# Kernel tuning notes

Measured on AMD Instinct MI355X. Metric: run time of the kernel, lower is better.

The kernel has to match this reference:

```python
import jax, jax.numpy as jnp
import numpy as np
import math

B, S, D = 16, 2048, 128
MASK_SENTINEL = -100

def setup_inputs() -> dict:
    key = jax.random.key(0)
    k1, k2, k3, k4 = jax.random.split(key, 4)
    value = jax.random.normal(k1, (B, S, D), dtype=jnp.float32)
    key_t = jax.random.normal(k2, (B, S, D), dtype=jnp.float32)
    query = jax.random.normal(k3, (B, S, D), dtype=jnp.float32)
    # mask uses -100 as the "masked out" sentinel, anything else is kept.
    bits = jax.random.randint(k4, (B, S, S), 0, 2, dtype=jnp.int32)
    mask = jnp.where(bits == 0, jnp.int32(MASK_SENTINEL), jnp.int32(0))
    return {"value": value, "key": key_t, "query": query, "mask": mask}

def reference(value, key, query, mask):
    # scores: [B, Sq, Sk]
    scale = 1.0 / math.sqrt(query.shape[-1])
    scores = jnp.einsum("bqd,bkd->bqk", query, key) * scale
    min_val = jnp.finfo(scores.dtype).min
    masked = jnp.where(mask == MASK_SENTINEL, min_val, scores)
    attn = jax.nn.softmax(masked, axis=-1)
    return jnp.einsum("bqk,bkd->bqd", attn, value)
```

## Files before the change

kernel.cpp:

```cpp
#include <hip/hip_runtime.h>
#include <hip/hip_bf16.h>

#define BATCH 16
#define SEQ   2048
#define DIM   128
#define QBLK  64
#define KVBLK 64
#define NT    (SEQ / KVBLK)
#define PPAD  72
#define L2E   1.4426950408889634f
#define THR   8.0f
#define MSENT -100

typedef __attribute__((ext_vector_type(8))) short bf16x8;
typedef __attribute__((ext_vector_type(4))) short bf16x4;
typedef __attribute__((ext_vector_type(4))) float f32x4;
typedef __attribute__((ext_vector_type(4))) unsigned u32x4;

__device__ __forceinline__ unsigned short f2bf(float f) {
  union { float f; unsigned u; } v; v.f = f;
  return (unsigned short)((v.u + 0x7FFFu + ((v.u >> 16) & 1u)) >> 16);
}
__device__ __forceinline__ unsigned packbf(float a, float b) {
  return ((unsigned)f2bf(b) << 16) | (unsigned)f2bf(a);
}

__global__ __launch_bounds__(256) void cvt_k(const float* __restrict__ K,
                                             short* __restrict__ Kb) {
  const size_t i = ((size_t)blockIdx.x * 256 + threadIdx.x) * 8;
  f32x4 a = __builtin_nontemporal_load((const f32x4*)(K + i));
  f32x4 b = __builtin_nontemporal_load((const f32x4*)(K + i + 4));
  u32x4 o = { packbf(a[0], a[1]), packbf(a[2], a[3]),
              packbf(b[0], b[1]), packbf(b[2], b[3]) };
  *(u32x4*)(Kb + i) = o;
}

__global__ __launch_bounds__(256) void cvt_vt(const float* __restrict__ V,
                                              short* __restrict__ Vt) {
  __shared__ unsigned t32[64][65];
  const int tid = threadIdx.x;
  const int b  = blockIdx.x >> 5;
  const int s0 = (blockIdx.x & 31) * 64;
  #pragma unroll
  for (int it = 0; it < 8; ++it) {
    const int idx = tid + it * 256;
    const int r = idx >> 5, c4 = idx & 31;
    f32x4 x = __builtin_nontemporal_load(
        (const f32x4*)(V + ((size_t)b * SEQ + s0 + r) * DIM + c4 * 4));
    t32[r][c4 * 2]     = packbf(x[0], x[1]);
    t32[r][c4 * 2 + 1] = packbf(x[2], x[3]);
  }
  __syncthreads();
  const int d = tid >> 1, sh = tid & 1;
  unsigned short outv[32];
  #pragma unroll
  for (int j = 0; j < 32; ++j) {
    const unsigned u = t32[sh * 32 + j][d >> 1];
    outv[j] = (d & 1) ? (unsigned short)(u >> 16) : (unsigned short)(u & 0xffff);
  }
  short* op = Vt + ((size_t)b * DIM + d) * SEQ + s0 + sh * 32;
  #pragma unroll
  for (int q = 0; q < 4; ++q) {
    bf16x8 y;
    #pragma unroll
    for (int j = 0; j < 8; ++j) y[j] = (short)outv[q * 8 + j];
    *(bf16x8*)(op + q * 8) = y;
  }
}

__device__ __forceinline__ void gload16(const void* g, void* l) {
  __builtin_amdgcn_global_load_lds(
      (const __attribute__((address_space(1))) unsigned*)g,
      (__attribute__((address_space(3))) unsigned*)l, 16, 0, 0);
}

__device__ __forceinline__ void stage_kv(const char* __restrict__ Kb2,
                                         const char* __restrict__ Vtb2,
                                         int k0, int w, int l,
                                         short* kbuf, short* vbuf) {
  #pragma unroll
  for (int it = 0; it < 4; ++it) {
    const int ch = w * 4 + it;
    const int r  = ch * 4 + (l >> 4);
    const int cs = ((l & 15) * 16) ^ ((r & 7) << 4);
    gload16(Kb2 + (size_t)(k0 + r) * 256 + cs, (char*)kbuf + ch * 1024);
  }
  #pragma unroll
  for (int it = 0; it < 4; ++it) {
    const int ch = w * 4 + it;
    const int d  = ch * 8 + (l >> 3);
    const int cs = ((l & 7) * 16) ^ ((d & 7) << 4);
    gload16(Vtb2 + (size_t)d * (SEQ * 2) + k0 * 2 + cs, (char*)vbuf + ch * 1024);
  }
}

__global__ __launch_bounds__(256, 2) void attn_fwd(
    const short* __restrict__ Kbf, const short* __restrict__ Vt,
    const float* __restrict__ Qg, const int* __restrict__ Mg,
    float* __restrict__ Og) {
  __shared__ short lds_k[2][KVBLK * DIM];
  __shared__ short lds_v[2][DIM * KVBLK];
  __shared__ short lds_p[4][16 * PPAD];

  const int tid = threadIdx.x;
  const int w   = tid >> 6;
  const int l   = tid & 63;
  const int g   = l >> 4;
  const int lr  = l & 15;

  const int blk = blockIdx.x;
  const int b   = blk >> 5;
  const int q0  = (blk & 31) * QBLK;

  const float scale = 0.08838834764831845f;

  const char* Kb2  = (const char*)(Kbf + (size_t)b * SEQ * DIM);
  const char* Vtb2 = (const char*)(Vt  + (size_t)b * DIM * SEQ);
  const int*  Mb   = Mg + (size_t)b * SEQ * SEQ;
  const int* const Mrow[4] = {
    Mb + (size_t)(q0 + w * 16 + 4 * g + 0) * SEQ + lr,
    Mb + (size_t)(q0 + w * 16 + 4 * g + 1) * SEQ + lr,
    Mb + (size_t)(q0 + w * 16 + 4 * g + 2) * SEQ + lr,
    Mb + (size_t)(q0 + w * 16 + 4 * g + 3) * SEQ + lr };

  stage_kv(Kb2, Vtb2, 0, w, l, lds_k[0], lds_v[0]);
  int mreg[16];
  #pragma unroll
  for (int sub = 0; sub < 4; ++sub)
    #pragma unroll
    for (int i = 0; i < 4; ++i)
      mreg[sub * 4 + i] = __builtin_nontemporal_load(Mrow[i] + sub * 16);

  bf16x8 qa[4];
  {
    const float* qbase = Qg + ((size_t)b * SEQ + (size_t)(q0 + w * 16 + lr)) * DIM + g * 8;
    #pragma unroll
    for (int kk = 0; kk < 4; ++kk) {
      f32x4 x0 = *(const f32x4*)(qbase + kk * 32);
      f32x4 x1 = *(const f32x4*)(qbase + kk * 32 + 4);
      bf16x8 f;
      #pragma unroll
      for (int j = 0; j < 4; ++j) {
        f[j]     = (short)f2bf(x0[j] * scale);
        f[j + 4] = (short)f2bf(x1[j] * scale);
      }
      qa[kk] = f;
    }
  }

  f32x4 acc[8];
  #pragma unroll
  for (int t = 0; t < 8; ++t) acc[t] = (f32x4){0.f, 0.f, 0.f, 0.f};
  float mrow[4] = {-1e30f, -1e30f, -1e30f, -1e30f};
  float lsum[4] = {0.f, 0.f, 0.f, 0.f};

  __syncthreads();
  int cur = 0;

  for (int t = 0; t < NT; ++t) {
    const int k0 = t * KVBLK;
    if (t + 1 < NT)
      stage_kv(Kb2, Vtb2, k0 + KVBLK, w, l, lds_k[cur ^ 1], lds_v[cur ^ 1]);

    const char* kbuf = (const char*)lds_k[cur];
    const char* vbuf = (const char*)lds_v[cur];

    f32x4 s[4];
    #pragma unroll
    for (int sub = 0; sub < 4; ++sub) {
      f32x4 sv = (f32x4){0.f, 0.f, 0.f, 0.f};
      const int krow = sub * 16 + lr;
      #pragma unroll
      for (int kk = 0; kk < 4; ++kk) {
        const int cb = (kk * 64 + g * 16) ^ ((krow & 7) << 4);
        bf16x8 kb = *(const bf16x8*)(kbuf + krow * 256 + cb);
        sv = __builtin_amdgcn_mfma_f32_16x16x32_bf16(qa[kk], kb, sv, 0, 0, 0);
      }
      s[sub] = sv;
    }

    #pragma unroll
    for (int sub = 0; sub < 4; ++sub)
      #pragma unroll
      for (int i = 0; i < 4; ++i)
        if (mreg[sub * 4 + i] == MSENT) s[sub][i] = -1e30f;
    if (t + 1 < NT) {
      #pragma unroll
      for (int sub = 0; sub < 4; ++sub)
        #pragma unroll
        for (int i = 0; i < 4; ++i)
          mreg[sub * 4 + i] =
              __builtin_nontemporal_load(Mrow[i] + k0 + KVBLK + sub * 16);
    }

    float tmax[4];
    bool chg = false;
    #pragma unroll
    for (int i = 0; i < 4; ++i) {
      float tm = fmaxf(fmaxf(s[0][i], s[1][i]), fmaxf(s[2][i], s[3][i]));
      #pragma unroll
      for (int dlt = 1; dlt < 16; dlt <<= 1)
        tm = fmaxf(tm, __shfl_xor(tm, dlt, 16));
      tmax[i] = tm;
      chg = chg || (tm > mrow[i] + THR);
    }
    if (__any(chg)) {
      #pragma unroll
      for (int i = 0; i < 4; ++i) {
        const float mnew = fmaxf(mrow[i], tmax[i]);
        const float alpha = __builtin_amdgcn_exp2f((mrow[i] - mnew) * L2E);
        mrow[i] = mnew;
        lsum[i] *= alpha;
        #pragma unroll
        for (int t8 = 0; t8 < 8; ++t8) acc[t8][i] *= alpha;
      }
    }

    #pragma unroll
    for (int sub = 0; sub < 4; ++sub)
      #pragma unroll
      for (int i = 0; i < 4; ++i) {
        const float p = __builtin_amdgcn_exp2f((s[sub][i] - mrow[i]) * L2E);
        lsum[i] += p;
        lds_p[w][(4 * g + i) * PPAD + sub * 16 + lr] = (short)f2bf(p);
      }

    bf16x8 pa[2];
    #pragma unroll
    for (int kk = 0; kk < 2; ++kk)
      pa[kk] = *(const bf16x8*)&lds_p[w][lr * PPAD + kk * 32 + g * 8];
    #pragma unroll
    for (int t8 = 0; t8 < 8; ++t8) {
      const int d = 16 * t8 + lr;
      #pragma unroll
      for (int kk = 0; kk < 2; ++kk) {
        const int cb = (kk * 64 + g * 16) ^ ((d & 7) << 4);
        bf16x8 vb = *(const bf16x8*)(vbuf + d * 128 + cb);
        acc[t8] = __builtin_amdgcn_mfma_f32_16x16x32_bf16(pa[kk], vb, acc[t8], 0, 0, 0);
      }
    }

    __syncthreads();
    cur ^= 1;
  }

  float rden[4];
  #pragma unroll
  for (int i = 0; i < 4; ++i) {
    float sm = lsum[i];
    #pragma unroll
    for (int dlt = 1; dlt < 16; dlt <<= 1) sm += __shfl_xor(sm, dlt, 16);
    rden[i] = 1.f / sm;
  }
  float* ob = Og + ((size_t)b * SEQ + (size_t)(q0 + w * 16)) * DIM;
  #pragma unroll
  for (int t8 = 0; t8 < 8; ++t8)
    #pragma unroll
    for (int i = 0; i < 4; ++i)
      ob[(4 * g + i) * DIM + 16 * t8 + lr] = acc[t8][i] * rden[i];
}

extern "C" void kernel_launch(void* const* d_in, const int* in_sizes, int n_in,
                              void* d_out, int out_size, void* d_ws, size_t ws_size,
                              hipStream_t stream) {
  (void)in_sizes; (void)n_in; (void)out_size; (void)ws_size;
  const float* Vg = (const float*)d_in[0];
  const float* Kg = (const float*)d_in[1];
  const float* Qg = (const float*)d_in[2];
  const int*   Mg = (const int*)d_in[3];
  float* Og = (float*)d_out;

  short* Kbf = (short*)d_ws;
  short* Vt  = Kbf + (size_t)BATCH * SEQ * DIM;
  cvt_k<<<dim3(BATCH * SEQ * DIM / (8 * 256)), 256, 0, stream>>>(Kg, Kbf);
  cvt_vt<<<dim3(BATCH * (SEQ / 64)), 256, 0, stream>>>(Vg, Vt);
  attn_fwd<<<dim3(BATCH * (SEQ / QBLK)), 256, 0, stream>>>(Kbf, Vt, Qg, Mg, Og);
}
```

Baseline: 118.4 us.

## Transpose QK^T MFMA, vectorize mask loads, new LDS swizzle, block remap, finer waits

```diff
diff --git a/kernel.cpp b/kernel.cpp
--- a/kernel.cpp
+++ b/kernel.cpp
@@ -13,8 +13,8 @@
 #define MSENT -100
 
 typedef __attribute__((ext_vector_type(8))) short bf16x8;
-typedef __attribute__((ext_vector_type(4))) short bf16x4;
 typedef __attribute__((ext_vector_type(4))) float f32x4;
+typedef __attribute__((ext_vector_type(4))) int   i32x4;
 typedef __attribute__((ext_vector_type(4))) unsigned u32x4;
 
 __device__ __forceinline__ unsigned short f2bf(float f) {
@@ -77,20 +77,23 @@
 __device__ __forceinline__ void stage_kv(const char* __restrict__ Kb2,
                                          const char* __restrict__ Vtb2,
                                          int k0, int w, int l,
-                                         short* kbuf, short* vbuf) {
+                                         void* kbuf, void* vbuf) {
   #pragma unroll
   for (int it = 0; it < 4; ++it) {
     const int ch = w * 4 + it;
     const int r  = ch * 4 + (l >> 4);
-    const int cs = ((l & 15) * 16) ^ ((r & 7) << 4);
-    gload16(Kb2 + (size_t)(k0 + r) * 256 + cs, (char*)kbuf + ch * 1024);
+    const int sg = (l & 15) ^ (r & 15);
+    gload16(Kb2 + (size_t)(k0 + r) * 256 + sg * 16, (char*)kbuf + ch * 1024);
   }
   #pragma unroll
   for (int it = 0; it < 4; ++it) {
     const int ch = w * 4 + it;
-    const int d  = ch * 8 + (l >> 3);
-    const int cs = ((l & 7) * 16) ^ ((d & 7) << 4);
-    gload16(Vtb2 + (size_t)d * (SEQ * 2) + k0 * 2 + cs, (char*)vbuf + ch * 1024);
+    const int d2 = ch * 4 + (l >> 4);
+    const int Su = (l & 15) ^ (d2 & 15);
+    const int d  = 2 * d2 + (Su >> 3);
+    const int m  = Su & 7;
+    gload16(Vtb2 + (size_t)d * (SEQ * 2) + k0 * 2 + m * 16,
+            (char*)vbuf + ch * 1024);
   }
 }
 
@@ -109,27 +112,18 @@
   const int lr  = l & 15;
 
   const int blk = blockIdx.x;
-  const int b   = blk >> 5;
-  const int q0  = (blk & 31) * QBLK;
+  const int swz = (blk & 7) * 64 + (blk >> 3);
+  const int b   = swz >> 5;
+  const int q0  = (swz & 31) * QBLK;
 
   const float scale = 0.08838834764831845f;
 
   const char* Kb2  = (const char*)(Kbf + (size_t)b * SEQ * DIM);
   const char* Vtb2 = (const char*)(Vt  + (size_t)b * DIM * SEQ);
-  const int*  Mb   = Mg + (size_t)b * SEQ * SEQ;
-  const int* const Mrow[4] = {
-    Mb + (size_t)(q0 + w * 16 + 4 * g + 0) * SEQ + lr,
-    Mb + (size_t)(q0 + w * 16 + 4 * g + 1) * SEQ + lr,
-    Mb + (size_t)(q0 + w * 16 + 4 * g + 2) * SEQ + lr,
-    Mb + (size_t)(q0 + w * 16 + 4 * g + 3) * SEQ + lr };
+  const int*  Mr   = Mg + (size_t)b * SEQ * SEQ + (size_t)(q0 + w * 16 + lr) * SEQ;
 
   stage_kv(Kb2, Vtb2, 0, w, l, lds_k[0], lds_v[0]);
-  int mreg[16];
-  #pragma unroll
-  for (int sub = 0; sub < 4; ++sub)
-    #pragma unroll
-    for (int i = 0; i < 4; ++i)
-      mreg[sub * 4 + i] = __builtin_nontemporal_load(Mrow[i] + sub * 16);
+  __builtin_amdgcn_sched_barrier(0);
 
   bf16x8 qa[4];
   {
@@ -147,83 +141,90 @@
       qa[kk] = f;
     }
   }
+  __builtin_amdgcn_sched_barrier(0);
+
+  i32x4 mreg[4];
+  #pragma unroll
+  for (int sub = 0; sub < 4; ++sub)
+    mreg[sub] = __builtin_nontemporal_load((const i32x4*)(Mr + 16 * sub + 4 * g));
 
   f32x4 acc[8];
   #pragma unroll
   for (int t = 0; t < 8; ++t) acc[t] = (f32x4){0.f, 0.f, 0.f, 0.f};
-  float mrow[4] = {-1e30f, -1e30f, -1e30f, -1e30f};
-  float lsum[4] = {0.f, 0.f, 0.f, 0.f};
-
-  __syncthreads();
+  float mrow = -1e30f, lsum = 0.f;
+
+  asm volatile("s_waitcnt vmcnt(4)" ::: "memory");
+  __builtin_amdgcn_s_barrier();
+
   int cur = 0;
-
   for (int t = 0; t < NT; ++t) {
     const int k0 = t * KVBLK;
     if (t + 1 < NT)
       stage_kv(Kb2, Vtb2, k0 + KVBLK, w, l, lds_k[cur ^ 1], lds_v[cur ^ 1]);
+    __builtin_amdgcn_sched_barrier(0);
 
     const char* kbuf = (const char*)lds_k[cur];
     const char* vbuf = (const char*)lds_v[cur];
 
     f32x4 s[4];
     #pragma unroll
-    for (int sub = 0; sub < 4; ++sub) {
-      f32x4 sv = (f32x4){0.f, 0.f, 0.f, 0.f};
-      const int krow = sub * 16 + lr;
-      #pragma unroll
-      for (int kk = 0; kk < 4; ++kk) {
-        const int cb = (kk * 64 + g * 16) ^ ((krow & 7) << 4);
+    for (int sub = 0; sub < 4; ++sub) s[sub] = (f32x4){0.f, 0.f, 0.f, 0.f};
+    #pragma unroll
+    for (int kk = 0; kk < 4; ++kk) {
+      #pragma unroll
+      for (int sub = 0; sub < 4; ++sub) {
+        const int krow = sub * 16 + lr;
+        const int cb = (64 * kk + 16 * g) ^ (lr << 4);
         bf16x8 kb = *(const bf16x8*)(kbuf + krow * 256 + cb);
-        sv = __builtin_amdgcn_mfma_f32_16x16x32_bf16(qa[kk], kb, sv, 0, 0, 0);
-      }
-      s[sub] = sv;
+        s[sub] = __builtin_amdgcn_mfma_f32_16x16x32_bf16(kb, qa[kk], s[sub], 0, 0, 0);
+      }
     }
 
     #pragma unroll
     for (int sub = 0; sub < 4; ++sub)
       #pragma unroll
       for (int i = 0; i < 4; ++i)
-        if (mreg[sub * 4 + i] == MSENT) s[sub][i] = -1e30f;
+        if (mreg[sub][i] == MSENT) s[sub][i] = -1e30f;
     if (t + 1 < NT) {
       #pragma unroll
       for (int sub = 0; sub < 4; ++sub)
+        mreg[sub] = __builtin_nontemporal_load(
+            (const i32x4*)(Mr + k0 + KVBLK + 16 * sub + 4 * g));
+    }
+
+    float tm = -1e30f;
+    #pragma unroll
+    for (int sub = 0; sub < 4; ++sub)
+      #pragma unroll
+      for (int i = 0; i < 4; ++i) tm = fmaxf(tm, s[sub][i]);
+    tm = fmaxf(tm, __shfl_xor(tm, 16));
+    tm = fmaxf(tm, __shfl_xor(tm, 32));
+    if (__any(tm > mrow + THR)) {
+      const float mnew = fmaxf(mrow, tm);
+      const float al = __builtin_amdgcn_exp2f((mrow - mnew) * L2E);
+      mrow = mnew; lsum *= al;
+      float av[4];
+      #pragma unroll
+      for (int i = 0; i < 4; ++i) av[i] = __shfl(al, 4 * g + i);
+      #pragma unroll
+      for (int t8 = 0; t8 < 8; ++t8)
         #pragma unroll
-        for (int i = 0; i < 4; ++i)
-          mreg[sub * 4 + i] =
-              __builtin_nontemporal_load(Mrow[i] + k0 + KVBLK + sub * 16);
-    }
-
-    float tmax[4];
-    bool chg = false;
-    #pragma unroll
-    for (int i = 0; i < 4; ++i) {
-      float tm = fmaxf(fmaxf(s[0][i], s[1][i]), fmaxf(s[2][i], s[3][i]));
-      #pragma unroll
-      for (int dlt = 1; dlt < 16; dlt <<= 1)
-        tm = fmaxf(tm, __shfl_xor(tm, dlt, 16));
-      tmax[i] = tm;
-      chg = chg || (tm > mrow[i] + THR);
-    }
-    if (__any(chg)) {
-      #pragma unroll
-      for (int i = 0; i < 4; ++i) {
-        const float mnew = fmaxf(mrow[i], tmax[i]);
-        const float alpha = __builtin_amdgcn_exp2f((mrow[i] - mnew) * L2E);
-        mrow[i] = mnew;
-        lsum[i] *= alpha;
-        #pragma unroll
-        for (int t8 = 0; t8 < 8; ++t8) acc[t8][i] *= alpha;
-      }
-    }
-
-    #pragma unroll
-    for (int sub = 0; sub < 4; ++sub)
-      #pragma unroll
-      for (int i = 0; i < 4; ++i) {
-        const float p = __builtin_amdgcn_exp2f((s[sub][i] - mrow[i]) * L2E);
-        lsum[i] += p;
-        lds_p[w][(4 * g + i) * PPAD + sub * 16 + lr] = (short)f2bf(p);
-      }
+        for (int i = 0; i < 4; ++i) acc[t8][i] *= av[i];
+    }
+
+    {
+      unsigned* prow = (unsigned*)&lds_p[w][lr * PPAD];
+      #pragma unroll
+      for (int sub = 0; sub < 4; ++sub) {
+        const float p0 = __builtin_amdgcn_exp2f((s[sub][0] - mrow) * L2E);
+        const float p1 = __builtin_amdgcn_exp2f((s[sub][1] - mrow) * L2E);
+        const float p2 = __builtin_amdgcn_exp2f((s[sub][2] - mrow) * L2E);
+        const float p3 = __builtin_amdgcn_exp2f((s[sub][3] - mrow) * L2E);
+        lsum += (p0 + p1) + (p2 + p3);
+        prow[8 * sub + 2 * g]     = packbf(p0, p1);
+        prow[8 * sub + 2 * g + 1] = packbf(p2, p3);
+      }
+    }
 
     bf16x8 pa[2];
     #pragma unroll
@@ -231,33 +232,34 @@
       pa[kk] = *(const bf16x8*)&lds_p[w][lr * PPAD + kk * 32 + g * 8];
     #pragma unroll
     for (int t8 = 0; t8 < 8; ++t8) {
-      const int d = 16 * t8 + lr;
+      const int d2 = 8 * t8 + (lr >> 1);
       #pragma unroll
       for (int kk = 0; kk < 2; ++kk) {
-        const int cb = (kk * 64 + g * 16) ^ ((d & 7) << 4);
-        bf16x8 vb = *(const bf16x8*)(vbuf + d * 128 + cb);
+        const int S = ((lr & 1) * 8 + 4 * kk + g) ^ (d2 & 15);
+        bf16x8 vb = *(const bf16x8*)(vbuf + d2 * 256 + S * 16);
         acc[t8] = __builtin_amdgcn_mfma_f32_16x16x32_bf16(pa[kk], vb, acc[t8], 0, 0, 0);
       }
     }
 
-    __syncthreads();
+    if (t + 1 < NT) {
+      asm volatile("s_waitcnt vmcnt(4)" ::: "memory");
+      __builtin_amdgcn_s_barrier();
+    }
     cur ^= 1;
   }
 
-  float rden[4];
-  #pragma unroll
-  for (int i = 0; i < 4; ++i) {
-    float sm = lsum[i];
-    #pragma unroll
-    for (int dlt = 1; dlt < 16; dlt <<= 1) sm += __shfl_xor(sm, dlt, 16);
-    rden[i] = 1.f / sm;
-  }
+  lsum += __shfl_xor(lsum, 16);
+  lsum += __shfl_xor(lsum, 32);
+  const float rden = 1.f / lsum;
+  float rdv[4];
+  #pragma unroll
+  for (int i = 0; i < 4; ++i) rdv[i] = __shfl(rden, 4 * g + i);
   float* ob = Og + ((size_t)b * SEQ + (size_t)(q0 + w * 16)) * DIM;
   #pragma unroll
   for (int t8 = 0; t8 < 8; ++t8)
     #pragma unroll
     for (int i = 0; i < 4; ++i)
-      ob[(4 * g + i) * DIM + 16 * t8 + lr] = acc[t8][i] * rden[i];
+      ob[(4 * g + i) * DIM + 16 * t8 + lr] = acc[t8][i] * rdv[i];
 }
 
 extern "C" void kernel_launch(void* const* d_in, const int* in_sizes, int n_in,
```

Result: no change. 117.3 us (-0.9%).
